# Performance work log

Hardware: AMD Instinct MI355X
Metric: run time of the kernel (lower is better)

Reference implementation:

```python
import jax, jax.numpy as jnp
import numpy as np

NEG_SLOPE = 0.2  # PyG GATConv leaky_relu slope


def gat_conv(x, src, dst, W, a_src, a_dst, bias, heads, out_ch, concat, n_nodes):
    # x: [N, in], W: [heads*out_ch, in], a_src/a_dst: [heads, out_ch]
    h = (x @ W.T).reshape(n_nodes, heads, out_ch)          # [N,H,C]
    alpha_src = (h * a_src).sum(-1)                         # [N,H]
    alpha_dst = (h * a_dst).sum(-1)                         # [N,H]
    e = jax.nn.leaky_relu(alpha_src[src] + alpha_dst[dst], NEG_SLOPE)  # [E,H]
    # segment softmax over incoming edges of each dst node (self-loops ensure non-empty)
    m = jax.ops.segment_max(e, dst, num_segments=n_nodes)
    e = jnp.exp(e - m[dst])
    s = jax.ops.segment_sum(e, dst, num_segments=n_nodes)
    alpha = e / (s[dst] + 1e-16)                            # [E,H]
    msg = h[src] * alpha[:, :, None]                        # [E,H,C]
    out = jax.ops.segment_sum(msg, dst, num_segments=n_nodes)  # [N,H,C]
    out = out.reshape(n_nodes, heads * out_ch) if concat else out.mean(axis=1)
    return out + bias


def setup_inputs() -> dict:
    key = jax.random.key(0)
    ks = jax.random.split(key, 16)
    N, E, IN, HID, OUT, H1, H2 = 10000, 160000, 256, 32, 32, 8, 10
    inp = {
        "x": jax.random.normal(ks[0], (N, IN), dtype=jnp.float32),
        "edge_index": jax.random.randint(ks[1], (2, E), 0, N, dtype=jnp.int64),
        # GATConv 1: in=256 -> 8 heads x 32
        "W1": jax.random.normal(ks[2], (H1 * HID, IN), dtype=jnp.float32) * 0.05,
        "a1s": jax.random.normal(ks[3], (H1, HID), dtype=jnp.float32) * 0.05,
        "a1d": jax.random.normal(ks[4], (H1, HID), dtype=jnp.float32) * 0.05,
        "b1": jnp.zeros((H1 * HID,), dtype=jnp.float32),
        # GATConv 2: in=256 -> 8 heads x 32
        "W2": jax.random.normal(ks[5], (H1 * HID, H1 * HID), dtype=jnp.float32) * 0.05,
        "a2s": jax.random.normal(ks[6], (H1, HID), dtype=jnp.float32) * 0.05,
        "a2d": jax.random.normal(ks[7], (H1, HID), dtype=jnp.float32) * 0.05,
        "b2": jnp.zeros((H1 * HID,), dtype=jnp.float32),
        # GATConv 3: in=256 -> 10 heads x 32, concat=False (mean)
        "W3": jax.random.normal(ks[8], (H2 * OUT, H1 * HID), dtype=jnp.float32) * 0.05,
        "a3s": jax.random.normal(ks[9], (H2, OUT), dtype=jnp.float32) * 0.05,
        "a3d": jax.random.normal(ks[10], (H2, OUT), dtype=jnp.float32) * 0.05,
        "b3": jnp.zeros((OUT,), dtype=jnp.float32),
        # residual projections
        "P1W": jax.random.normal(ks[11], (H1 * HID, IN), dtype=jnp.float32) * 0.05,
        "P1b": jnp.zeros((H1 * HID,), dtype=jnp.float32),
        "P3W": jax.random.normal(ks[12], (OUT, H1 * HID), dtype=jnp.float32) * 0.05,
        "P3b": jnp.zeros((OUT,), dtype=jnp.float32),
    }
    return inp


def reference(x, edge_index, W1, a1s, a1d, b1, W2, a2s, a2d, b2,
              W3, a3s, a3d, b3, P1W, P1b, P3W, P3b):
    N = x.shape[0]
    loop = jnp.arange(N, dtype=edge_index.dtype)
    src = jnp.concatenate([edge_index[0], loop])  # PyG adds self-loops by default
    dst = jnp.concatenate([edge_index[1], loop])

    identity1 = x @ P1W.T + P1b
    h = gat_conv(x, src, dst, W1, a1s, a1d, b1, 8, 32, True, N)
    h = jax.nn.elu(h) + identity1  # dropout inactive in eval

    identity2 = h
    h2 = gat_conv(h, src, dst, W2, a2s, a2d, b2, 8, 32, True, N)
    h = jax.nn.elu(h2) + identity2

    identity3 = h @ P3W.T + P3b
    h3 = gat_conv(h, src, dst, W3, a3s, a3d, b3, 10, 32, False, N)
    return h3 + identity3
```

## Files before the change

### kernel.cpp

```cpp
#include <hip/hip_runtime.h>
#include <hip/hip_bf16.h>

typedef __hip_bfloat16 bf16;
typedef __attribute__((ext_vector_type(8))) short bf16x8;
typedef __attribute__((ext_vector_type(4))) short bf16x4;
typedef __attribute__((ext_vector_type(4))) float f32x4;


static __device__ __forceinline__ float bf2f(bf16 v) { return __bfloat162float(v); }
static __device__ __forceinline__ float bf2fs(short v) {
    unsigned int u = ((unsigned int)(unsigned short)v) << 16;
    return __builtin_bit_cast(float, u);
}
static __device__ __forceinline__ short f2bfs(float f) {
    bf16 b = __float2bfloat16(f);
    return __builtin_bit_cast(short, b);
}
static __device__ __forceinline__ float loadf(const void* p, size_t i, int isf32) {
    return isf32 ? ((const float*)p)[i] : bf2f(((const bf16*)p)[i]);
}
static __device__ __forceinline__ int get_isf32(const int* flags) {
    return (flags[0] | (flags[2] == 0)) ? 1 : 0;
}

__global__ void k_zero(int* __restrict__ flags, int* __restrict__ cnt, int N) {
    int i = blockIdx.x * blockDim.x + threadIdx.x;
    if (i < 4) flags[i] = 0;
    for (; i < N; i += gridDim.x * blockDim.x) cnt[i] = 0;
}

__global__ void k_detect(const unsigned short* __restrict__ xu, const int* __restrict__ ew,
                         int* __restrict__ flags, int nx, int ne2, int bx) {
    __shared__ int lf[3];
    if (threadIdx.x < 3) lf[threadIdx.x] = 0;
    __syncthreads();
    if ((int)blockIdx.x < bx) {
        for (int i = blockIdx.x * 256 + threadIdx.x; i < nx; i += bx * 256) {
            unsigned short v = xu[i];
            if ((v & 0x7F80u) == 0x7F80u) lf[0] = 1;
            if (((i & 1) == 0) && v != 0) lf[2] = 1;
        }
    } else {
        int nb = gridDim.x - bx;
        for (int i = (blockIdx.x - bx) * 256 + threadIdx.x; i < ne2; i += nb * 256) {
            if ((i & 1) && ew[i] != 0) lf[1] = 1;
        }
    }
    __syncthreads();
    if (threadIdx.x == 0) {
        if (lf[0]) atomicOr(&flags[0], 1);
        if (lf[1]) atomicOr(&flags[1], 1);
        if (lf[2]) atomicOr(&flags[2], 1);
    }
}

static __device__ __forceinline__ void cast8(const void* src, bf16* dst, int i8, int isf32) {
    if (isf32) {
        f32x4 a = ((const f32x4*)src)[2 * i8];
        f32x4 b = ((const f32x4*)src)[2 * i8 + 1];
        bf16x8 o;
        o[0] = f2bfs(a[0]); o[1] = f2bfs(a[1]); o[2] = f2bfs(a[2]); o[3] = f2bfs(a[3]);
        o[4] = f2bfs(b[0]); o[5] = f2bfs(b[1]); o[6] = f2bfs(b[2]); o[7] = f2bfs(b[3]);
        ((bf16x8*)dst)[i8] = o;
    } else {
        ((bf16x8*)dst)[i8] = ((const bf16x8*)src)[i8];
    }
}

__global__ void k_cast_norm(const void* s0, bf16* d0, int c0,
                            const void* s1, bf16* d1, int c1,
                            const void* s2, bf16* d2, int c2,
                            const void* s3, bf16* d3, int c3,
                            const void* s4, bf16* d4, int c4,
                            const void* s5, bf16* d5, int c5,
                            const int* __restrict__ w, int* __restrict__ es,
                            int* __restrict__ ed, int* __restrict__ cnt, int E,
                            const int* __restrict__ flags, int cb) {
    if ((int)blockIdx.x < cb) {
        int t = blockIdx.x * 256 + threadIdx.x;
        int isf32 = get_isf32(flags);
        if (t < c0) { cast8(s0, d0, t, isf32); return; } t -= c0;
        if (t < c1) { cast8(s1, d1, t, isf32); return; } t -= c1;
        if (t < c2) { cast8(s2, d2, t, isf32); return; } t -= c2;
        if (t < c3) { cast8(s3, d3, t, isf32); return; } t -= c3;
        if (t < c4) { cast8(s4, d4, t, isf32); return; } t -= c4;
        if (t < c5) { cast8(s5, d5, t, isf32); }
    } else {
        int e = (blockIdx.x - cb) * 256 + threadIdx.x;
        if (e >= E) return;
        int sv, dv;
        if (flags[1] == 0) {
            sv = w[2 * (size_t)e];
            dv = w[2 * (size_t)E + 2 * (size_t)e];
        } else {
            sv = w[e];
            dv = w[(size_t)E + e];
        }
        es[e] = sv;
        ed[e] = dv;
        atomicAdd(&cnt[dv], 1);
    }
}

__global__ void k_scan(int* __restrict__ cnt, int* __restrict__ row_ptr, int N) {
    __shared__ int part[1024];
    int tid = threadIdx.x;
    int vpt = (N + 1023) >> 10;
    int i0 = tid * vpt;
    int i1 = i0 + vpt; if (i1 > N) i1 = N;
    int s = 0;
    for (int i = i0; i < i1; ++i) s += cnt[i] + 1;
    part[tid] = s;
    __syncthreads();
    for (int off = 1; off < 1024; off <<= 1) {
        int t = (tid >= off) ? part[tid - off] : 0;
        __syncthreads();
        part[tid] += t;
        __syncthreads();
    }
    int run = (tid == 0) ? 0 : part[tid - 1];
    for (int i = i0; i < i1; ++i) {
        int c = cnt[i] + 1;
        cnt[i] = run;
        run += c;
        row_ptr[i + 1] = run;
    }
    if (tid == 0) row_ptr[0] = 0;
}

__global__ void k_fill(const int* __restrict__ edst, int* __restrict__ cursor,
                       const int* __restrict__ row_ptr, int* __restrict__ csr_e,
                       int E, int N) {
    int e = blockIdx.x * blockDim.x + threadIdx.x;
    if (e < E) {
        int d = edst[e];
        int pos = atomicAdd(&cursor[d], 1);
        csr_e[pos] = e;
    } else if (e < E + N) {
        int d = e - E;
        csr_e[row_ptr[d + 1] - 1] = e;
    }
}

template<int NT>
__global__ void k_gemm_split(const bf16* __restrict__ A, const bf16* __restrict__ W,
                             const void* __restrict__ bias1, const int* __restrict__ flags,
                             bf16* __restrict__ out0, int S0, int ld0,
                             bf16* __restrict__ out1, int ld1, int n1,
                             int M, int Fo, int K,
                             const void* __restrict__ aS, const void* __restrict__ aD,
                             float* __restrict__ asrc, float* __restrict__ adst, int H) {
    int wid = threadIdx.x >> 6;
    int lane = threadIdx.x & 63;
    int mrow = blockIdx.x * 64 + wid * 16;
    if (mrow >= M) return;
    int ncol = blockIdx.y * (NT * 16);
    int r = lane & 15, g = lane >> 4;

    f32x4 acc[NT];
#pragma unroll
    for (int t = 0; t < NT; ++t) acc[t] = (f32x4){0.f, 0.f, 0.f, 0.f};

    const bf16* arow = A + (size_t)(mrow + r) * K + g * 8;
    const bf16* wbase = W + (size_t)(ncol + r) * K + g * 8;
    for (int k0 = 0; k0 < K; k0 += 32) {
        bf16x8 af = *(const bf16x8*)(arow + k0);
#pragma unroll
        for (int t = 0; t < NT; ++t) {
            bf16x8 bfr = *(const bf16x8*)(wbase + (size_t)t * 16 * K + k0);
            acc[t] = __builtin_amdgcn_mfma_f32_16x16x32_bf16(af, bfr, acc[t], 0, 0, 0);
        }
    }
    int isf32 = get_isf32(flags);

#pragma unroll
    for (int t = 0; t < NT; ++t) {
        int n = ncol + t * 16 + r;
        bool is0 = n < S0;
        int jc = n - S0;
        float bv = (!is0 && jc < n1 && bias1) ? loadf(bias1, jc, isf32) : 0.f;
#pragma unroll
        for (int j = 0; j < 4; ++j) {
            int m = mrow + 4 * g + j;
            float v = acc[t][j] + bv;
            if (is0) out0[(size_t)m * ld0 + n] = __float2bfloat16(v);
            else if (jc < n1) out1[(size_t)m * ld1 + jc] = __float2bfloat16(v);
        }
    }

    if (aS && ncol < S0) {
        float ps[2][4], pd[2][4];
#pragma unroll
        for (int hb = 0; hb < 2; ++hb)
#pragma unroll
            for (int j = 0; j < 4; ++j) { ps[hb][j] = 0.f; pd[hb][j] = 0.f; }
#pragma unroll
        for (int t = 0; t < NT; ++t) {
            int col = ncol + t * 16 + r;
            float asv = loadf(aS, col, isf32);
            float adv = loadf(aD, col, isf32);
#pragma unroll
            for (int j = 0; j < 4; ++j) {
                ps[t >> 1][j] += acc[t][j] * asv;
                pd[t >> 1][j] += acc[t][j] * adv;
            }
        }
#pragma unroll
        for (int mk = 1; mk <= 8; mk <<= 1) {
#pragma unroll
            for (int hb = 0; hb < 2; ++hb)
#pragma unroll
                for (int j = 0; j < 4; ++j) {
                    ps[hb][j] += __shfl_xor(ps[hb][j], mk);
                    pd[hb][j] += __shfl_xor(pd[hb][j], mk);
                }
        }
        if (r == 0) {
            int hA = ncol >> 5, hB = hA + 1;
#pragma unroll
            for (int j = 0; j < 4; ++j) {
                int m = mrow + 4 * g + j;
                asrc[(size_t)m * H + hA] = ps[0][j];
                asrc[(size_t)m * H + hB] = ps[1][j];
                adst[(size_t)m * H + hA] = pd[0][j];
                adst[(size_t)m * H + hB] = pd[1][j];
            }
        }
    }
}

#define CAP 96
__global__ void k_fused_agg(const bf16* __restrict__ hlin,
                            const float* __restrict__ asrc, const float* __restrict__ adst,
                            const int* __restrict__ esrc, const int* __restrict__ row_ptr,
                            const int* __restrict__ csr_e,
                            const void* __restrict__ bias, const bf16* __restrict__ identb,
                            void* __restrict__ out, bf16* __restrict__ outb,
                            const int* __restrict__ flags,
                            int E, int N, int H, int mode) {
    __shared__ float el[4][CAP * 10];
    __shared__ int   ssrc[4][CAP];
    __shared__ float idn[4][10];
    int wid = threadIdx.x >> 6, lane = threadIdx.x & 63;
    int d = blockIdx.x * 4 + wid;
    bool active = d < N;
    int isf32 = get_isf32(flags);
    int F = H * 32;
    int nj = (F + 255) >> 8;
    int lo = 0, deg = 0;
    if (active) { lo = row_ptr[d]; deg = row_ptr[d + 1] - lo; }
    bool fast = deg <= CAP;

    if (active && fast) {
        int EC = 64 / H;
        int h = lane % H, ei = lane / H;
        float ad = adst[(size_t)d * H + h];
        for (int base = 0; base < deg; base += EC) {
            int p = base + ei;
            if (ei < EC && p < deg) {
                int e = csr_e[lo + p];
                int s = (e < E) ? esrc[e] : (e - E);
                float v = asrc[(size_t)s * H + h] + ad;
                v = (v > 0.f) ? v : 0.2f * v;
                el[wid][p * H + h] = v;
                if (h == 0) ssrc[wid][p] = s;
            }
        }
    }
    __syncthreads();
    if (active && fast) {
        if (H == 8) {
            int h = lane & 7, sub = lane >> 3;
            float m = -1e30f;
            for (int p = sub; p < deg; p += 8) m = fmaxf(m, el[wid][p * 8 + h]);
            m = fmaxf(m, __shfl_xor(m, 8));
            m = fmaxf(m, __shfl_xor(m, 16));
            m = fmaxf(m, __shfl_xor(m, 32));
            float den = 0.f;
            for (int p = sub; p < deg; p += 8) {
                float t = __expf(el[wid][p * 8 + h] - m);
                el[wid][p * 8 + h] = t;
                den += t;
            }
            den += __shfl_xor(den, 8);
            den += __shfl_xor(den, 16);
            den += __shfl_xor(den, 32);
            if (lane < 8) idn[wid][lane] = 1.f / (den + 1e-16f);
        } else if (lane < H) {
            float m = -1e30f;
            for (int p = 0; p < deg; ++p) m = fmaxf(m, el[wid][p * H + lane]);
            float den = 0.f;
            for (int p = 0; p < deg; ++p) {
                float t = __expf(el[wid][p * H + lane] - m);
                el[wid][p * H + lane] = t;
                den += t;
            }
            idn[wid][lane] = 1.f / (den + 1e-16f);
        }
    }
    __syncthreads();
    if (!active) return;

    if (mode == 1 && fast) {
        int g = lane & 15, q = lane >> 4;
        int f0 = g * 16;
        f32x4 a0 = {0.f,0.f,0.f,0.f}, a1 = {0.f,0.f,0.f,0.f};
        f32x4 a2 = {0.f,0.f,0.f,0.f}, a3 = {0.f,0.f,0.f,0.f};
        int p = q;
        for (; p + 4 < deg; p += 8) {
            int s0 = ssrc[wid][p];
            int s1 = ssrc[wid][p + 4];
            const bf16* hp0 = hlin + (size_t)s0 * 256 + f0;
            const bf16* hp1 = hlin + (size_t)s1 * 256 + f0;
            bf16x8 u0 = *(const bf16x8*)hp0;
            bf16x8 u1 = *(const bf16x8*)(hp0 + 8);
            bf16x8 v0 = *(const bf16x8*)hp1;
            bf16x8 v1 = *(const bf16x8*)(hp1 + 8);
            float w0 = el[wid][p * 8 + (g >> 1)];
            float w1 = el[wid][(p + 4) * 8 + (g >> 1)];
#pragma unroll
            for (int k = 0; k < 4; ++k) {
                a0[k] += w0 * bf2fs(u0[k]);
                a1[k] += w0 * bf2fs(u0[4 + k]);
                a2[k] += w0 * bf2fs(u1[k]);
                a3[k] += w0 * bf2fs(u1[4 + k]);
                a0[k] += w1 * bf2fs(v0[k]);
                a1[k] += w1 * bf2fs(v0[4 + k]);
                a2[k] += w1 * bf2fs(v1[k]);
                a3[k] += w1 * bf2fs(v1[4 + k]);
            }
        }
        if (p < deg) {
            int s0 = ssrc[wid][p];
            const bf16* hp0 = hlin + (size_t)s0 * 256 + f0;
            bf16x8 u0 = *(const bf16x8*)hp0;
            bf16x8 u1 = *(const bf16x8*)(hp0 + 8);
            float w0 = el[wid][p * 8 + (g >> 1)];
#pragma unroll
            for (int k = 0; k < 4; ++k) {
                a0[k] += w0 * bf2fs(u0[k]);
                a1[k] += w0 * bf2fs(u0[4 + k]);
                a2[k] += w0 * bf2fs(u1[k]);
                a3[k] += w0 * bf2fs(u1[4 + k]);
            }
        }
#pragma unroll
        for (int k = 0; k < 4; ++k) {
            a0[k] += __shfl_xor(a0[k], 16); a1[k] += __shfl_xor(a1[k], 16);
            a2[k] += __shfl_xor(a2[k], 16); a3[k] += __shfl_xor(a3[k], 16);
            a0[k] += __shfl_xor(a0[k], 32); a1[k] += __shfl_xor(a1[k], 32);
            a2[k] += __shfl_xor(a2[k], 32); a3[k] += __shfl_xor(a3[k], 32);
        }
        if (lane < 16) {
            float inv = idn[wid][g >> 1];
            const bf16* idp = identb + (size_t)d * 256 + f0;
            bf16x8 id0 = *(const bf16x8*)idp;
            bf16x8 id1 = *(const bf16x8*)(idp + 8);
            bf16* ob = outb + (size_t)d * 256 + f0;
            f32x4 av[4] = {a0, a1, a2, a3};
            bf16x8 obv0, obv1;
#pragma unroll
            for (int i = 0; i < 4; ++i) {
#pragma unroll
                for (int k = 0; k < 4; ++k) {
                    float v = av[i][k] * inv + loadf(bias, f0 + 4 * i + k, isf32);
                    v = (v > 0.f) ? v : (__expf(v) - 1.f);
                    int e8 = 4 * i + k;
                    v += bf2fs((e8 < 8) ? id0[e8] : id1[e8 - 8]);
                    if (i < 2) obv0[e8] = f2bfs(v);
                    else       obv1[e8 - 8] = f2bfs(v);
                }
            }
            *(bf16x8*)ob = obv0;
            *(bf16x8*)(ob + 8) = obv1;
        }
        return;
    }

    if (mode == 2 && fast) {
        int g = lane & 15, q = lane >> 4;
        int f0 = g * 16;
        int f1 = 256 + g * 4;
        f32x4 a0 = {0.f,0.f,0.f,0.f}, a1 = {0.f,0.f,0.f,0.f};
        f32x4 a2 = {0.f,0.f,0.f,0.f}, a3 = {0.f,0.f,0.f,0.f};
        f32x4 a4 = {0.f,0.f,0.f,0.f};
        int p = q;
        for (; p + 4 < deg; p += 8) {
            int s0 = ssrc[wid][p];
            int s1 = ssrc[wid][p + 4];
            const bf16* hp0 = hlin + (size_t)s0 * 320;
            const bf16* hp1 = hlin + (size_t)s1 * 320;
            bf16x8 u0 = *(const bf16x8*)(hp0 + f0);
            bf16x8 u1 = *(const bf16x8*)(hp0 + f0 + 8);
            bf16x4 u2 = *(const bf16x4*)(hp0 + f1);
            bf16x8 v0 = *(const bf16x8*)(hp1 + f0);
            bf16x8 v1 = *(const bf16x8*)(hp1 + f0 + 8);
            bf16x4 v2 = *(const bf16x4*)(hp1 + f1);
            float w00 = el[wid][p * 10 + (g >> 1)];
            float w02 = el[wid][p * 10 + 8 + (g >> 3)];
            float w10 = el[wid][(p + 4) * 10 + (g >> 1)];
            float w12 = el[wid][(p + 4) * 10 + 8 + (g >> 3)];
#pragma unroll
            for (int k = 0; k < 4; ++k) {
                a0[k] += w00 * bf2fs(u0[k]);
                a1[k] += w00 * bf2fs(u0[4 + k]);
                a2[k] += w00 * bf2fs(u1[k]);
                a3[k] += w00 * bf2fs(u1[4 + k]);
                a4[k] += w02 * bf2fs(u2[k]);
                a0[k] += w10 * bf2fs(v0[k]);
                a1[k] += w10 * bf2fs(v0[4 + k]);
                a2[k] += w10 * bf2fs(v1[k]);
                a3[k] += w10 * bf2fs(v1[4 + k]);
                a4[k] += w12 * bf2fs(v2[k]);
            }
        }
        if (p < deg) {
            int s0 = ssrc[wid][p];
            const bf16* hp0 = hlin + (size_t)s0 * 320;
            bf16x8 u0 = *(const bf16x8*)(hp0 + f0);
            bf16x8 u1 = *(const bf16x8*)(hp0 + f0 + 8);
            bf16x4 u2 = *(const bf16x4*)(hp0 + f1);
            float w00 = el[wid][p * 10 + (g >> 1)];
            float w02 = el[wid][p * 10 + 8 + (g >> 3)];
#pragma unroll
            for (int k = 0; k < 4; ++k) {
                a0[k] += w00 * bf2fs(u0[k]);
                a1[k] += w00 * bf2fs(u0[4 + k]);
                a2[k] += w00 * bf2fs(u1[k]);
                a3[k] += w00 * bf2fs(u1[4 + k]);
                a4[k] += w02 * bf2fs(u2[k]);
            }
        }
#pragma unroll
        for (int k = 0; k < 4; ++k) {
            a0[k] += __shfl_xor(a0[k], 16); a1[k] += __shfl_xor(a1[k], 16);
            a2[k] += __shfl_xor(a2[k], 16); a3[k] += __shfl_xor(a3[k], 16);
            a4[k] += __shfl_xor(a4[k], 16);
            a0[k] += __shfl_xor(a0[k], 32); a1[k] += __shfl_xor(a1[k], 32);
            a2[k] += __shfl_xor(a2[k], 32); a3[k] += __shfl_xor(a3[k], 32);
            a4[k] += __shfl_xor(a4[k], 32);
        }
        float* scratch = &el[wid][0];
        if (lane < 16) {
            float inv0 = idn[wid][g >> 1];
            float inv2 = idn[wid][8 + (g >> 3)];
#pragma unroll
            for (int k = 0; k < 4; ++k) {
                scratch[f0 + k]      = a0[k] * inv0;
                scratch[f0 + 4 + k]  = a1[k] * inv0;
                scratch[f0 + 8 + k]  = a2[k] * inv0;
                scratch[f0 + 12 + k] = a3[k] * inv0;
                scratch[f1 + k]      = a4[k] * inv2;
            }
        }
        if (lane < 32) {
            float s = 0.f;
#pragma unroll
            for (int h = 0; h < 10; ++h) s += scratch[h * 32 + lane];
            float v = s * 0.1f + loadf(bias, lane, isf32)
                    + bf2f(identb[(size_t)d * 32 + lane]);
            if (isf32) ((float*)out)[(size_t)d * 32 + lane] = v;
            else ((bf16*)out)[(size_t)d * 32 + lane] = __float2bfloat16(v);
        }
        return;
    }

    f32x4 acc[2] = {(f32x4){0.f,0.f,0.f,0.f}, (f32x4){0.f,0.f,0.f,0.f}};
    for (int j = 0; j < nj; ++j) {
        int f0 = (lane + 64 * j) * 4;
        if (f0 >= F) continue;
        int hj = f0 >> 5;
        float ad = adst[(size_t)d * H + hj];
        float m = -1e30f;
        for (int p = 0; p < deg; ++p) {
            int e = csr_e[lo + p];
            int s = (e < E) ? esrc[e] : (e - E);
            float v = asrc[(size_t)s * H + hj] + ad;
            v = (v > 0.f) ? v : 0.2f * v;
            m = fmaxf(m, v);
        }
        float den = 0.f;
        f32x4 a4 = {0.f, 0.f, 0.f, 0.f};
        for (int p = 0; p < deg; ++p) {
            int e = csr_e[lo + p];
            int s = (e < E) ? esrc[e] : (e - E);
            float v = asrc[(size_t)s * H + hj] + ad;
            v = (v > 0.f) ? v : 0.2f * v;
            float t = __expf(v - m);
            den += t;
            bf16x4 hv = *(const bf16x4*)(hlin + (size_t)s * F + f0);
            for (int k = 0; k < 4; ++k) a4[k] += t * bf2fs(hv[k]);
        }
        float inv = 1.f / (den + 1e-16f);
        for (int k = 0; k < 4; ++k) acc[j][k] = a4[k] * inv;
    }
    if (mode == 1) {
        int f0 = lane * 4;
        bf16x4 ob;
#pragma unroll
        for (int k = 0; k < 4; ++k) {
            float v = acc[0][k] + loadf(bias, f0 + k, isf32);
            v = (v > 0.f) ? v : (__expf(v) - 1.f);
            v += bf2f(identb[(size_t)d * F + f0 + k]);
            ob[k] = f2bfs(v);
        }
        *(bf16x4*)(outb + (size_t)d * F + f0) = ob;
    } else {
        float* scratch = &el[wid][0];
#pragma unroll
        for (int j = 0; j < 2; ++j) {
            int f0 = (lane + 64 * j) * 4;
            if (j < nj && f0 < F) {
#pragma unroll
                for (int k = 0; k < 4; ++k) scratch[f0 + k] = acc[j][k];
            }
        }
        if (lane < 32) {
            float s = 0.f;
            for (int h = 0; h < H; ++h) s += scratch[h * 32 + lane];
            float v = s * (1.f / (float)H) + loadf(bias, lane, isf32)
                    + bf2f(identb[(size_t)d * 32 + lane]);
            if (isf32) ((float*)out)[(size_t)d * 32 + lane] = v;
            else ((bf16*)out)[(size_t)d * 32 + lane] = __float2bfloat16(v);
        }
    }
}

extern "C" void kernel_launch(void* const* d_in, const int* in_sizes, int n_in,
                              void* d_out, int out_size, void* d_ws, size_t ws_size,
                              hipStream_t stream) {
    const int IN = 256, C = 32;
    const int N = in_sizes[0] / IN;
    const int E = in_sizes[1] / 2;
    const int ET = E + N;

    const void* x    = d_in[0];
    const int*  edge = (const int*)d_in[1];
    const void* W1 = d_in[2];
    const void* a1s = d_in[3];
    const void* a1d = d_in[4];
    const void* b1 = d_in[5];
    const void* W2 = d_in[6];
    const void* a2s = d_in[7];
    const void* a2d = d_in[8];
    const void* b2 = d_in[9];
    const void* W3 = d_in[10];
    const void* a3s = d_in[11];
    const void* a3d = d_in[12];
    const void* b3 = d_in[13];
    const void* P1W = d_in[14];
    const void* P1b = d_in[15];
    const void* P3W = d_in[16];
    const void* P3b = d_in[17];

    char* ws = (char*)d_ws;
    size_t off = 0;
    auto alloc = [&](size_t bytes) -> void* {
        void* p = ws + off;
        off = (off + bytes + 255) & ~(size_t)255;
        return p;
    };
    bf16* fxb   = (bf16*)alloc((size_t)N * 256 * 2);
    bf16* fyb   = (bf16*)alloc((size_t)N * 256 * 2);
    bf16* fhb   = (bf16*)alloc((size_t)N * 320 * 2);
    bf16* fidb  = (bf16*)alloc((size_t)N * 256 * 2);
    float* fasrc = (float*)alloc((size_t)N * 10 * 4);
    float* fadst = (float*)alloc((size_t)N * 10 * 4);
    bf16* wc1   = (bf16*)alloc((size_t)512 * 256 * 2);
    bf16* wb2   = (bf16*)alloc((size_t)256 * 256 * 2);
    bf16* wc3   = (bf16*)alloc((size_t)384 * 256 * 2);
    int*  isrc  = (int*)alloc((size_t)E * 4);
    int*  idst  = (int*)alloc((size_t)E * 4);
    int*  irow  = (int*)alloc((size_t)(N + 1) * 4);
    int*  icur  = (int*)alloc((size_t)N * 4);
    int*  icsr  = (int*)alloc((size_t)ET * 4);
    int*  flags = (int*)alloc(4 * 4);
    (void)ws_size;

    auto cdiv = [](int a, int b) { return (a + b - 1) / b; };

    k_zero<<<cdiv(N, 256), 256, 0, stream>>>(flags, icur, N);

    int nprobe_x = (N * 256 < 16384) ? N * 256 : 16384;
    int nprobe_e = (2 * E < 8192) ? 2 * E : 8192;
    int bx = cdiv(nprobe_x, 256) < 16 ? cdiv(nprobe_x, 256) : 16;
    int be = cdiv(nprobe_e, 256) < 8 ? cdiv(nprobe_e, 256) : 8;
    k_detect<<<bx + be, 256, 0, stream>>>(
        (const unsigned short*)x, edge, flags, nprobe_x, nprobe_e, bx);

    int c_x = N * 256 / 8, c_w = 256 * 256 / 8, c_w3 = 320 * 256 / 8, c_p3 = 32 * 256 / 8;
    int ctot = c_x + 3 * c_w + c_w3 + c_p3;
    int cb = cdiv(ctot, 256);
    k_cast_norm<<<cb + cdiv(E, 256), 256, 0, stream>>>(
        x, fxb, c_x,
        W1, wc1, c_w,
        P1W, wc1 + (size_t)256 * 256, c_w,
        W2, wb2, c_w,
        W3, wc3, c_w3,
        P3W, wc3 + (size_t)320 * 256, c_p3,
        edge, isrc, idst, icur, E, flags, cb);

    k_scan<<<1, 1024, 0, stream>>>(icur, irow, N);
    k_fill<<<cdiv(ET, 256), 256, 0, stream>>>(idst, icur, irow, icsr, E, N);

    int gx = cdiv(N, 64);
    int ga = cdiv(N, 4);

    {
        int H = 8;
        k_gemm_split<4><<<dim3(gx, 8), 256, 0, stream>>>(
            fxb, wc1, P1b, flags, fhb, 256, 256, fidb, 256, 256, N, 512, 256,
            a1s, a1d, fasrc, fadst, H);
        k_fused_agg<<<ga, 256, 0, stream>>>(fhb, fasrc, fadst, isrc, irow, icsr,
                                            b1, fidb, nullptr, fyb, flags, E, N, H, 1);
    }
    {
        int H = 8;
        k_gemm_split<4><<<dim3(gx, 4), 256, 0, stream>>>(
            fyb, wb2, nullptr, flags, fhb, 256, 256, nullptr, 0, 0, N, 256, 256,
            a2s, a2d, fasrc, fadst, H);
        k_fused_agg<<<ga, 256, 0, stream>>>(fhb, fasrc, fadst, isrc, irow, icsr,
                                            b2, fyb, nullptr, fyb, flags, E, N, H, 1);
    }
    {
        int H = 10;
        k_gemm_split<4><<<dim3(gx, 6), 256, 0, stream>>>(
            fyb, wc3, P3b, flags, fhb, 320, 320, fidb, 32, 32, N, 384, 256,
            a3s, a3d, fasrc, fadst, H);
        k_fused_agg<<<ga, 256, 0, stream>>>(fhb, fasrc, fadst, isrc, irow, icsr,
                                            b3, fidb, d_out, nullptr, flags, E, N, H, 2);
    }
}
```

Measured before the change: 201.7 us.

## Replace block barriers with wave LDS fences, skip x cast, unroll GEMM K

Each wave in the aggregation kernel handles its own destination node and only touches its own LDS slice, so the block-wide __syncthreads are replaced by an lgkmcnt wait, and inactive waves return early. When the input is already bf16, the GEMM reads x directly and the cast kernel skips copying it. The GEMM K dimension becomes a template constant so the loop can be fully unrolled. Together these cut barrier stalls, one copy pass and loop overhead. The risk is that relying on a waitcnt alone for intra-wave LDS visibility could be fragile.

```diff
diff --git a/kernel.cpp b/kernel.cpp
--- a/kernel.cpp
+++ b/kernel.cpp
@@ -21,6 +21,9 @@
 }
 static __device__ __forceinline__ int get_isf32(const int* flags) {
     return (flags[0] | (flags[2] == 0)) ? 1 : 0;
+}
+static __device__ __forceinline__ void wave_lds_fence() {
+    asm volatile("s_waitcnt lgkmcnt(0)" ::: "memory");
 }
 
 __global__ void k_zero(int* __restrict__ flags, int* __restrict__ cnt, int N) {
@@ -79,7 +82,7 @@
     if ((int)blockIdx.x < cb) {
         int t = blockIdx.x * 256 + threadIdx.x;
         int isf32 = get_isf32(flags);
-        if (t < c0) { cast8(s0, d0, t, isf32); return; } t -= c0;
+        if (t < c0) { if (isf32) cast8(s0, d0, t, 1); return; } t -= c0;
         if (t < c1) { cast8(s1, d1, t, isf32); return; } t -= c1;
         if (t < c2) { cast8(s2, d2, t, isf32); return; } t -= c2;
         if (t < c3) { cast8(s3, d3, t, isf32); return; } t -= c3;
@@ -142,18 +145,21 @@
     }
 }
 
-template<int NT>
-__global__ void k_gemm_split(const bf16* __restrict__ A, const bf16* __restrict__ W,
+template<int NT, int KK>
+__global__ void k_gemm_split(const bf16* __restrict__ Acast, const void* __restrict__ Araw,
+                             const bf16* __restrict__ W,
                              const void* __restrict__ bias1, const int* __restrict__ flags,
                              bf16* __restrict__ out0, int S0, int ld0,
                              bf16* __restrict__ out1, int ld1, int n1,
-                             int M, int Fo, int K,
+                             int M, int Fo,
                              const void* __restrict__ aS, const void* __restrict__ aD,
                              float* __restrict__ asrc, float* __restrict__ adst, int H) {
     int wid = threadIdx.x >> 6;
     int lane = threadIdx.x & 63;
     int mrow = blockIdx.x * 64 + wid * 16;
     if (mrow >= M) return;
+    int isf32 = get_isf32(flags);
+    const bf16* A = (Araw && !isf32) ? (const bf16*)Araw : Acast;
     int ncol = blockIdx.y * (NT * 16);
     int r = lane & 15, g = lane >> 4;
 
@@ -161,17 +167,17 @@
 #pragma unroll
     for (int t = 0; t < NT; ++t) acc[t] = (f32x4){0.f, 0.f, 0.f, 0.f};
 
-    const bf16* arow = A + (size_t)(mrow + r) * K + g * 8;
-    const bf16* wbase = W + (size_t)(ncol + r) * K + g * 8;
-    for (int k0 = 0; k0 < K; k0 += 32) {
+    const bf16* arow = A + (size_t)(mrow + r) * KK + g * 8;
+    const bf16* wbase = W + (size_t)(ncol + r) * KK + g * 8;
+#pragma unroll
+    for (int k0 = 0; k0 < KK; k0 += 32) {
         bf16x8 af = *(const bf16x8*)(arow + k0);
 #pragma unroll
         for (int t = 0; t < NT; ++t) {
-            bf16x8 bfr = *(const bf16x8*)(wbase + (size_t)t * 16 * K + k0);
+            bf16x8 bfr = *(const bf16x8*)(wbase + (size_t)t * 16 * KK + k0);
             acc[t] = __builtin_amdgcn_mfma_f32_16x16x32_bf16(af, bfr, acc[t], 0, 0, 0);
         }
     }
-    int isf32 = get_isf32(flags);
 
 #pragma unroll
     for (int t = 0; t < NT; ++t) {
@@ -250,8 +256,9 @@
     int lo = 0, deg = 0;
     if (active) { lo = row_ptr[d]; deg = row_ptr[d + 1] - lo; }
     bool fast = deg <= CAP;
-
-    if (active && fast) {
+    if (!active) return;
+
+    if (fast) {
         int EC = 64 / H;
         int h = lane % H, ei = lane / H;
         float ad = adst[(size_t)d * H + h];
@@ -267,8 +274,8 @@
             }
         }
     }
-    __syncthreads();
-    if (active && fast) {
+    wave_lds_fence();
+    if (fast) {
         if (H == 8) {
             int h = lane & 7, sub = lane >> 3;
             float m = -1e30f;
@@ -298,8 +305,7 @@
             idn[wid][lane] = 1.f / (den + 1e-16f);
         }
     }
-    __syncthreads();
-    if (!active) return;
+    wave_lds_fence();
 
     if (mode == 1 && fast) {
         int g = lane & 15, q = lane >> 4;
@@ -453,6 +459,7 @@
                 scratch[f1 + k]      = a4[k] * inv2;
             }
         }
+        wave_lds_fence();
         if (lane < 32) {
             float s = 0.f;
 #pragma unroll
@@ -515,6 +522,7 @@
                 for (int k = 0; k < 4; ++k) scratch[f0 + k] = acc[j][k];
             }
         }
+        wave_lds_fence();
         if (lane < 32) {
             float s = 0.f;
             for (int h = 0; h < H; ++h) s += scratch[h * 32 + lane];
@@ -608,24 +616,24 @@
 
     {
         int H = 8;
-        k_gemm_split<4><<<dim3(gx, 8), 256, 0, stream>>>(
-            fxb, wc1, P1b, flags, fhb, 256, 256, fidb, 256, 256, N, 512, 256,
+        k_gemm_split<4, 256><<<dim3(gx, 8), 256, 0, stream>>>(
+            fxb, x, wc1, P1b, flags, fhb, 256, 256, fidb, 256, 256, N, 512,
             a1s, a1d, fasrc, fadst, H);
         k_fused_agg<<<ga, 256, 0, stream>>>(fhb, fasrc, fadst, isrc, irow, icsr,
                                             b1, fidb, nullptr, fyb, flags, E, N, H, 1);
     }
     {
         int H = 8;
-        k_gemm_split<4><<<dim3(gx, 4), 256, 0, stream>>>(
-            fyb, wb2, nullptr, flags, fhb, 256, 256, nullptr, 0, 0, N, 256, 256,
+        k_gemm_split<4, 256><<<dim3(gx, 4), 256, 0, stream>>>(
+            fyb, nullptr, wb2, nullptr, flags, fhb, 256, 256, nullptr, 0, 0, N, 256,
             a2s, a2d, fasrc, fadst, H);
         k_fused_agg<<<ga, 256, 0, stream>>>(fhb, fasrc, fadst, isrc, irow, icsr,
                                             b2, fyb, nullptr, fyb, flags, E, N, H, 1);
     }
     {
         int H = 10;
-        k_gemm_split<4><<<dim3(gx, 6), 256, 0, stream>>>(
-            fyb, wc3, P3b, flags, fhb, 320, 320, fidb, 32, 32, N, 384, 256,
+        k_gemm_split<4, 256><<<dim3(gx, 6), 256, 0, stream>>>(
+            fyb, nullptr, wc3, P3b, flags, fhb, 320, 320, fidb, 32, 32, N, 384,
             a3s, a3d, fasrc, fadst, H);
         k_fused_agg<<<ga, 256, 0, stream>>>(fhb, fasrc, fadst, isrc, irow, icsr,
                                             b3, fidb, d_out, nullptr, flags, E, N, H, 2);
```

Result: no change. 199.2 us (median of 2 runs) (-1.2%).
